# Optimization experiments

Hardware: AMD Instinct MI355X
Metric: run time of the kernel (lower is better)

## Reference

```python
import jax, jax.numpy as jnp
import numpy as np
from functools import partial

H = 51  # hidden size hard-coded in the module
B = 1024
T = 1024


def setup_inputs() -> dict:
    key = jax.random.key(0)
    ks = jax.random.split(key, 12)
    scale = 1.0 / np.sqrt(H)
    p = lambda k, shape: (jax.random.normal(k, shape, dtype=jnp.float32) * scale)
    return {
        "input": jax.random.normal(ks[0], (B, T), dtype=jnp.float32),
        # layer 1: LSTMCell(1, 51)
        "W_ih1": p(ks[1], (4 * H, 1)),
        "W_hh1": p(ks[2], (4 * H, H)),
        "b_ih1": p(ks[3], (4 * H,)),
        "b_hh1": p(ks[4], (4 * H,)),
        # layer 2: LSTMCell(51, 51)
        "W_ih2": p(ks[5], (4 * H, H)),
        "W_hh2": p(ks[6], (4 * H, H)),
        "b_ih2": p(ks[7], (4 * H,)),
        "b_hh2": p(ks[8], (4 * H,)),
        # Linear(51, 1)
        "W_lin": p(ks[9], (1, H)),
        "b_lin": p(ks[10], (1,)),
    }


def _lstm_cell(x, h, c, W_ih, W_hh, b_ih, b_hh):
    # PyTorch LSTMCell gate order: i, f, g, o
    gates = x @ W_ih.T + h @ W_hh.T + b_ih + b_hh  # [B, 4H]
    i, f, g, o = jnp.split(gates, 4, axis=-1)
    i = jax.nn.sigmoid(i)
    f = jax.nn.sigmoid(f)
    g = jnp.tanh(g)
    o = jax.nn.sigmoid(o)
    c_new = f * c + i * g
    h_new = o * jnp.tanh(c_new)
    return h_new, c_new


def reference(input, W_ih1, W_hh1, b_ih1, b_hh1, W_ih2, W_hh2, b_ih2, b_hh2, W_lin, b_lin):
    Bv = input.shape[0]
    dt = input.dtype
    init = (
        jnp.zeros((Bv, H), dt),  # h1
        jnp.zeros((Bv, H), dt),  # c1
        jnp.zeros((Bv, H), dt),  # h2
        jnp.zeros((Bv, H), dt),  # c2
    )

    def step(carry, x_t):  # x_t: [B, 1]
        h1, c1, h2, c2 = carry
        h1, c1 = _lstm_cell(x_t, h1, c1, W_ih1, W_hh1, b_ih1, b_hh1)
        h2, c2 = _lstm_cell(h1, h2, c2, W_ih2, W_hh2, b_ih2, b_hh2)
        y = h2 @ W_lin.T + b_lin  # [B, 1]
        return (h1, c1, h2, c2), y[:, 0]

    xs = input.T[:, :, None]  # [T, B, 1]
    _, ys = jax.lax.scan(step, init, xs)  # ys: [T, B]
    return ys.T  # [B, T]
```

## Files before the change

### kernel.cpp

```cpp
#include <hip/hip_runtime.h>


#define H     51
#define NROW  204
#define TLEN  1024
#define BPB   16
#define NTHR  896
#define NBLK  64
#define KPAD  88

#define LOG2E  1.442695041f
#define LOG2E2 2.885390082f

typedef __attribute__((ext_vector_type(8))) _Float16 half8;
typedef __attribute__((ext_vector_type(4))) float f4;

__device__ __forceinline__ float frcp(float x) { return __builtin_amdgcn_rcpf(x); }
#if __has_builtin(__builtin_amdgcn_exp2f)
__device__ __forceinline__ float ex2(float x) { return __builtin_amdgcn_exp2f(x); }
#else
__device__ __forceinline__ float ex2(float x) { return __expf(x * 0.6931471806f); }
#endif

__device__ __forceinline__ int posu(int u) {
    return (u & ~7) | ((u & 3) << 1) | ((u >> 2) & 1);
}
__device__ __forceinline__ int ipos(int p) {
    return (p & ~7) | ((p & 1) << 2) | ((p >> 1) & 3);
}

__device__ __forceinline__ half8 lds8h(const _Float16* p) {
    return *(const half8*)__builtin_assume_aligned(p, 16);
}

__device__ __forceinline__ void block_sync_lds() {
    asm volatile("s_waitcnt lgkmcnt(0)\n\ts_barrier" ::: "memory");
}

#define MFMA(ACC, A, B) \
    ACC = __builtin_amdgcn_mfma_f32_16x16x32_f16((A), (B), (ACC), 0, 0, 0)

__device__ __forceinline__ half8 load_wfrag(const float* __restrict__ W,
                                            int tile, int kt, int q, int mcol)
{
    half8 hf;
    const int prow = tile * 16 + mcol;
    const float sc = ((prow & 3) == 2) ? LOG2E2 : LOG2E;
#pragma unroll
    for (int j = 0; j < 8; ++j) {
        const int kk = ipos(kt * 32 + q * 8 + j);
        float v = 0.0f;
        if (prow < NROW && kk < H) {
            const int srow = (prow & 3) * H + (prow >> 2);
            v = W[srow * H + kk];
        }
        hf[j] = (_Float16)(v * sc);
    }
    return hf;
}

__device__ __forceinline__ float cell(float a_i, float a_f, float b_g,
                                      float d_o, float* c)
{
    const float e_i = ex2(-a_i);
    const float e_f = ex2(-a_f);
    const float Eg  = ex2(b_g);
    const float f   = frcp(1.0f + e_f);
    const float ig  = (Eg - 1.0f) * frcp((1.0f + e_i) * (Eg + 1.0f));
    const float cn  = fmaf(f, *c, ig);
    *c = cn;
    const float Ec  = ex2(cn * LOG2E2);
    const float e_o = ex2(-d_o);
    return (Ec - 1.0f) * frcp((Ec + 1.0f) * (1.0f + e_o));
}

__global__
__attribute__((amdgpu_flat_work_group_size(NTHR, NTHR), amdgpu_waves_per_eu(4, 4)))
void lstm2_kernel(const float* __restrict__ input,
                  const float* __restrict__ W_ih1, const float* __restrict__ W_hh1,
                  const float* __restrict__ b_ih1, const float* __restrict__ b_hh1,
                  const float* __restrict__ W_ih2, const float* __restrict__ W_hh2,
                  const float* __restrict__ b_ih2, const float* __restrict__ b_hh2,
                  const float* __restrict__ W_lin, const float* __restrict__ b_lin,
                  float* __restrict__ out)
{
    const int tid  = threadIdx.x;
    const int w    = tid >> 6;
    const int lane = tid & 63;
    const int q    = lane >> 4;
    const int mcol = lane & 15;
    const int b0   = blockIdx.x * BPB;

    const bool isL1 = (w < 7);
    const int  tw   = isL1 ? w : (w - 7);

    __shared__ __align__(16) _Float16 h1r[4][BPB][KPAD];
    __shared__ __align__(16) _Float16 h2r[2][BPB][KPAD];

    {
        _Float16* p1 = &h1r[0][0][0];
        for (int i = tid; i < 4 * BPB * KPAD; i += NTHR) p1[i] = (_Float16)0.0f;
        _Float16* p2 = &h2r[0][0][0];
        for (int i = tid; i < 2 * BPB * KPAD; i += NTHR) p2[i] = (_Float16)0.0f;
    }

    half8 Wa[2][2], Wb[2][2];
    f4 bbv[2], wxv[2];
    float cc[2] = {0.0f, 0.0f};
    int wp[2];
    const int tt[2] = {tw, 7 + tw};
#pragma unroll
    for (int s = 0; s < 2; ++s) {
        const int t = tt[s];
        const int u = 4 * t + q;
        wp[s] = posu(u);
#pragma unroll
        for (int kt = 0; kt < 2; ++kt) {
            if (isL1) {
                Wa[s][kt] = load_wfrag(W_hh1, t, kt, q, mcol);
            } else {
                Wa[s][kt] = load_wfrag(W_ih2, t, kt, q, mcol);
                Wb[s][kt] = load_wfrag(W_hh2, t, kt, q, mcol);
            }
        }
#pragma unroll
        for (int j = 0; j < 4; ++j) {
            const bool v = (t < 13) && (u < H);
            const float sc = (j == 2) ? LOG2E2 : LOG2E;
            if (isL1) {
                bbv[s][j] = v ? sc * (b_ih1[j * H + u] + b_hh1[j * H + u]) : 0.0f;
                wxv[s][j] = v ? sc * W_ih1[j * H + u] : 0.0f;
            } else {
                bbv[s][j] = v ? sc * (b_ih2[j * H + u] + b_hh2[j * H + u]) : 0.0f;
                wxv[s][j] = 0.0f;
            }
        }
    }

    float wl_a[8], wl_b[8];
    if (w == 7) {
#pragma unroll
        for (int j = 0; j < 8; ++j) {
            const int ra = ipos(q * 8 + j);
            const int rb = ipos(32 + q * 8 + j);
            wl_a[j] = (ra < H) ? W_lin[ra] : 0.0f;
            wl_b[j] = (rb < H) ? W_lin[rb] : 0.0f;
        }
    }
    const float blin = b_lin[0];

    float xcur = input[(size_t)(b0 + mcol) * TLEN + 0];
    half8 e1a = {0, 0, 0, 0, 0, 0, 0, 0};
    half8 e1b = {0, 0, 0, 0, 0, 0, 0, 0};

    __syncthreads();

#define STEP(KK, S1W, S1R, S2W, S2R, L1E, L2E, YE, ERE)                        \
do {                                                                           \
    const int k_ = (KK);                                                       \
    if (isL1) {                                                                \
        if (L1E) {                                                             \
            const int kn_ = (k_ + 1 < TLEN) ? (k_ + 1) : (TLEN - 1);           \
            const float xn_ = input[(size_t)(b0 + mcol) * TLEN + kn_];         \
            half8 B1a = lds8h(&h1r[S1R][mcol][q * 8]);                         \
            half8 B1b = lds8h(&h1r[S1R][mcol][32 + q * 8]);                    \
            f4 g0, g1;                                                         \
            g0[0] = fmaf(wxv[0][0], xcur, bbv[0][0]);                          \
            g0[1] = fmaf(wxv[0][1], xcur, bbv[0][1]);                          \
            g0[2] = fmaf(wxv[0][2], xcur, bbv[0][2]);                          \
            g0[3] = fmaf(wxv[0][3], xcur, bbv[0][3]);                          \
            g1[0] = fmaf(wxv[1][0], xcur, bbv[1][0]);                          \
            g1[1] = fmaf(wxv[1][1], xcur, bbv[1][1]);                          \
            g1[2] = fmaf(wxv[1][2], xcur, bbv[1][2]);                          \
            g1[3] = fmaf(wxv[1][3], xcur, bbv[1][3]);                          \
            MFMA(g0, Wa[0][0], B1a);  MFMA(g0, Wa[0][1], B1b);                 \
            MFMA(g1, Wa[1][0], B1a);  MFMA(g1, Wa[1][1], B1b);                 \
            const float h0 = cell(g0[0], g0[1], g0[2], g0[3], &cc[0]);         \
            const float h1v = cell(g1[0], g1[1], g1[2], g1[3], &cc[1]);        \
            h1r[S1W][mcol][wp[0]] = (_Float16)h0;                              \
            h1r[S1W][mcol][wp[1]] = (_Float16)h1v;                             \
            xcur = xn_;                                                        \
        }                                                                      \
    } else {                                                                   \
        if (L2E) {                                                             \
            half8 B2a = lds8h(&h2r[S2R][mcol][q * 8]);                         \
            half8 B2b = lds8h(&h2r[S2R][mcol][32 + q * 8]);                    \
            f4 g0 = bbv[0], g1 = bbv[1];                                       \
            MFMA(g0, Wa[0][0], e1a);  MFMA(g0, Wa[0][1], e1b);      \
            MFMA(g1, Wa[1][0], e1a);  MFMA(g1, Wa[1][1], e1b);                 \
            MFMA(g0, Wb[0][0], B2a);  MFMA(g0, Wb[0][1], B2b);                 \
            MFMA(g1, Wb[1][0], B2a);  MFMA(g1, Wb[1][1], B2b);                 \
            if (ERE) {             \
                e1a = lds8h(&h1r[S1R][mcol][q * 8]);                           \
                e1b = lds8h(&h1r[S1R][mcol][32 + q * 8]);                      \
            }                                                                  \
            const float h0 = cell(g0[0], g0[1], g0[2], g0[3], &cc[0]);         \
            const float h1v = cell(g1[0], g1[1], g1[2], g1[3], &cc[1]);        \
            h2r[S2W][mcol][wp[0]] = (_Float16)h0;                              \
            h2r[S2W][mcol][wp[1]] = (_Float16)h1v;                             \
            if ((YE) && w == 7) {    \
                float yp = 0.0f;                                               \
                _Pragma("unroll")                                              \
                for (int j = 0; j < 8; ++j) {                                  \
                    yp += wl_a[j] * (float)B2a[j];                             \
                    yp += wl_b[j] * (float)B2b[j];                             \
                }                                                              \
                yp += __shfl_xor(yp, 16);                                      \
                yp += __shfl_xor(yp, 32);                                      \
                if (q == 0) out[(size_t)(b0 + mcol) * TLEN + (k_ - 3)] = yp + blin; \
            }                                                                  \
        } else if (ERE) {                                                      \
            e1a = lds8h(&h1r[S1R][mcol][q * 8]);                               \
            e1b = lds8h(&h1r[S1R][mcol][32 + q * 8]);                          \
        }                                                                      \
    }                                                                          \
    block_sync_lds();                                                          \
} while (0)

    STEP(0, 0, 3, 0, 1, 1, 0, 0, 0);
    STEP(1, 1, 0, 1, 0, 1, 0, 0, 1);
    STEP(2, 2, 1, 0, 1, 1, 1, 0, 1);
    STEP(3, 3, 2, 1, 0, 1, 1, 1, 1);
    for (int k = 4; k <= 1020; k += 4) {
        STEP(k + 0, 0, 3, 0, 1, 1, 1, 1, 1);
        STEP(k + 1, 1, 0, 1, 0, 1, 1, 1, 1);
        STEP(k + 2, 2, 1, 0, 1, 1, 1, 1, 1);
        STEP(k + 3, 3, 2, 1, 0, 1, 1, 1, 1);
    }
    STEP(1024, 0, 3, 0, 1, 0, 1, 1, 1);
    STEP(1025, 1, 0, 1, 0, 0, 1, 1, 0);
#undef STEP

    if (w == 7) {
        half8 ya = lds8h(&h2r[1][mcol][q * 8]);
        half8 yb = lds8h(&h2r[1][mcol][32 + q * 8]);
        float yp = 0.0f;
#pragma unroll
        for (int j = 0; j < 8; ++j) {
            yp += wl_a[j] * (float)ya[j];
            yp += wl_b[j] * (float)yb[j];
        }
        yp += __shfl_xor(yp, 16);
        yp += __shfl_xor(yp, 32);
        if (q == 0) out[(size_t)(b0 + mcol) * TLEN + (TLEN - 1)] = yp + blin;
    }
}

extern "C" void kernel_launch(void* const* d_in, const int* in_sizes, int n_in,
                              void* d_out, int out_size, void* d_ws, size_t ws_size,
                              hipStream_t stream)
{
    const float* input = (const float*)d_in[0];
    const float* W_ih1 = (const float*)d_in[1];
    const float* W_hh1 = (const float*)d_in[2];
    const float* b_ih1 = (const float*)d_in[3];
    const float* b_hh1 = (const float*)d_in[4];
    const float* W_ih2 = (const float*)d_in[5];
    const float* W_hh2 = (const float*)d_in[6];
    const float* b_ih2 = (const float*)d_in[7];
    const float* b_hh2 = (const float*)d_in[8];
    const float* W_lin = (const float*)d_in[9];
    const float* b_lin = (const float*)d_in[10];

    float* out = (float*)d_out;

    hipLaunchKernelGGL(lstm2_kernel, dim3(NBLK), dim3(NTHR), 0, stream,
                       input, W_ih1, W_hh1, b_ih1, b_hh1,
                       W_ih2, W_hh2, b_ih2, b_hh2, W_lin, b_lin,
                       out);
}
```

Before: 724.2 us.

## Replace per-step block barriers with LDS counter flags between layer waves

Drops the block-wide barrier after every timestep. Layer-1 and layer-2 wave groups now signal progress through atomic counters in shared memory and spin with s_sleep until the data they need is ready. A 4-slot ring buffer for both hidden states lets layer 1 run up to a few steps ahead of layer 2, decoupling the two pipelines. This risks polling overhead, LDS atomic contention, and memory-ordering hazards, since writes are fenced only with lgkmcnt waits.

```diff
diff --git a/kernel.cpp b/kernel.cpp
--- a/kernel.cpp
+++ b/kernel.cpp
@@ -8,6 +8,7 @@
 #define NTHR  896
 #define NBLK  64
 #define KPAD  88
+#define RING  4
 
 #define LOG2E  1.442695041f
 #define LOG2E2 2.885390082f
@@ -31,10 +32,6 @@
 
 __device__ __forceinline__ half8 lds8h(const _Float16* p) {
     return *(const half8*)__builtin_assume_aligned(p, 16);
-}
-
-__device__ __forceinline__ void block_sync_lds() {
-    asm volatile("s_waitcnt lgkmcnt(0)\n\ts_barrier" ::: "memory");
 }
 
 #define MFMA(ACC, A, B) \
@@ -74,6 +71,14 @@
     return (Ec - 1.0f) * frcp((Ec + 1.0f) * (1.0f + e_o));
 }
 
+#define WAITGE(P, T)                                                           \
+do {                                                                           \
+    if (*(P) < (T)) {                                                          \
+        do { __builtin_amdgcn_s_sleep(1); } while (*(P) < (T));                \
+    }                                                                          \
+    __builtin_amdgcn_sched_barrier(0);                                         \
+} while (0)
+
 __global__
 __attribute__((amdgpu_flat_work_group_size(NTHR, NTHR), amdgpu_waves_per_eu(4, 4)))
 void lstm2_kernel(const float* __restrict__ input,
@@ -94,15 +99,19 @@
     const bool isL1 = (w < 7);
     const int  tw   = isL1 ? w : (w - 7);
 
-    __shared__ __align__(16) _Float16 h1r[4][BPB][KPAD];
-    __shared__ __align__(16) _Float16 h2r[2][BPB][KPAD];
+    __shared__ __align__(16) _Float16 h1r[RING][BPB][KPAD];
+    __shared__ __align__(16) _Float16 h2r[RING][BPB][KPAD];
+    __shared__ int dflag[16];
 
     {
         _Float16* p1 = &h1r[0][0][0];
-        for (int i = tid; i < 4 * BPB * KPAD; i += NTHR) p1[i] = (_Float16)0.0f;
+        for (int i = tid; i < RING * BPB * KPAD; i += NTHR) p1[i] = (_Float16)0.0f;
         _Float16* p2 = &h2r[0][0][0];
-        for (int i = tid; i < 2 * BPB * KPAD; i += NTHR) p2[i] = (_Float16)0.0f;
-    }
+        for (int i = tid; i < RING * BPB * KPAD; i += NTHR) p2[i] = (_Float16)0.0f;
+        if (tid < 16) dflag[tid] = 0;
+    }
+    volatile int* d1 = &dflag[0];
+    volatile int* d2 = &dflag[8];
 
     half8 Wa[2][2], Wb[2][2];
     f4 bbv[2], wxv[2];
@@ -149,101 +158,111 @@
     }
     const float blin = b_lin[0];
 
-    float xcur = input[(size_t)(b0 + mcol) * TLEN + 0];
-    half8 e1a = {0, 0, 0, 0, 0, 0, 0, 0};
-    half8 e1b = {0, 0, 0, 0, 0, 0, 0, 0};
+    float xcur = isL1 ? input[(size_t)(b0 + mcol) * TLEN + 0] : 0.0f;
 
     __syncthreads();
 
-#define STEP(KK, S1W, S1R, S2W, S2R, L1E, L2E, YE, ERE)                        \
+#define L1STEP(KK, SW, SR, W1, W2)                                             \
 do {                                                                           \
-    const int k_ = (KK);                                                       \
-    if (isL1) {                                                                \
-        if (L1E) {                                                             \
-            const int kn_ = (k_ + 1 < TLEN) ? (k_ + 1) : (TLEN - 1);           \
-            const float xn_ = input[(size_t)(b0 + mcol) * TLEN + kn_];         \
-            half8 B1a = lds8h(&h1r[S1R][mcol][q * 8]);                         \
-            half8 B1b = lds8h(&h1r[S1R][mcol][32 + q * 8]);                    \
-            f4 g0, g1;                                                         \
-            g0[0] = fmaf(wxv[0][0], xcur, bbv[0][0]);                          \
-            g0[1] = fmaf(wxv[0][1], xcur, bbv[0][1]);                          \
-            g0[2] = fmaf(wxv[0][2], xcur, bbv[0][2]);                          \
-            g0[3] = fmaf(wxv[0][3], xcur, bbv[0][3]);                          \
-            g1[0] = fmaf(wxv[1][0], xcur, bbv[1][0]);                          \
-            g1[1] = fmaf(wxv[1][1], xcur, bbv[1][1]);                          \
-            g1[2] = fmaf(wxv[1][2], xcur, bbv[1][2]);                          \
-            g1[3] = fmaf(wxv[1][3], xcur, bbv[1][3]);                          \
-            MFMA(g0, Wa[0][0], B1a);  MFMA(g0, Wa[0][1], B1b);                 \
-            MFMA(g1, Wa[1][0], B1a);  MFMA(g1, Wa[1][1], B1b);                 \
-            const float h0 = cell(g0[0], g0[1], g0[2], g0[3], &cc[0]);         \
-            const float h1v = cell(g1[0], g1[1], g1[2], g1[3], &cc[1]);        \
-            h1r[S1W][mcol][wp[0]] = (_Float16)h0;                              \
-            h1r[S1W][mcol][wp[1]] = (_Float16)h1v;                             \
-            xcur = xn_;                                                        \
+    const int k_  = (KK);                                                      \
+    const int kn_ = (k_ + 1 < TLEN) ? (k_ + 1) : (TLEN - 1);                   \
+    const float xn_ = input[(size_t)(b0 + mcol) * TLEN + kn_];                 \
+    if (W1) WAITGE(d1, 7 * k_);                                                \
+    if (W2) WAITGE(d2, 7 * (k_ - 3));                                          \
+    half8 B1a = lds8h(&h1r[SR][mcol][q * 8]);                                  \
+    half8 B1b = lds8h(&h1r[SR][mcol][32 + q * 8]);                             \
+    f4 g0, g1;                                                                 \
+    g0[0] = fmaf(wxv[0][0], xcur, bbv[0][0]);                                  \
+    g0[1] = fmaf(wxv[0][1], xcur, bbv[0][1]);                                  \
+    g0[2] = fmaf(wxv[0][2], xcur, bbv[0][2]);                                  \
+    g0[3] = fmaf(wxv[0][3], xcur, bbv[0][3]);                                  \
+    g1[0] = fmaf(wxv[1][0], xcur, bbv[1][0]);                                  \
+    g1[1] = fmaf(wxv[1][1], xcur, bbv[1][1]);                                  \
+    g1[2] = fmaf(wxv[1][2], xcur, bbv[1][2]);                                  \
+    g1[3] = fmaf(wxv[1][3], xcur, bbv[1][3]);                                  \
+    MFMA(g0, Wa[0][0], B1a);  MFMA(g0, Wa[0][1], B1b);                         \
+    MFMA(g1, Wa[1][0], B1a);  MFMA(g1, Wa[1][1], B1b);                         \
+    const float h0  = cell(g0[0], g0[1], g0[2], g0[3], &cc[0]);                \
+    const float h1v = cell(g1[0], g1[1], g1[2], g1[3], &cc[1]);                \
+    h1r[SW][mcol][wp[0]] = (_Float16)h0;                                       \
+    h1r[SW][mcol][wp[1]] = (_Float16)h1v;                                      \
+    asm volatile("s_waitcnt lgkmcnt(0)" ::: "memory");                         \
+    if (lane == 0) atomicAdd(&dflag[0], 1);                                    \
+    xcur = xn_;                                                                \
+} while (0)
+
+#define L2STEP(JJ, SW, SR2, W2, YE)                                            \
+do {                                                                           \
+    const int j_ = (JJ);                                                       \
+    WAITGE(d1, 7 * (j_ + 1));                                                  \
+    if (W2) WAITGE(d2, 7 * j_);                                                \
+    half8 B1a = lds8h(&h1r[SW][mcol][q * 8]);                                  \
+    half8 B1b = lds8h(&h1r[SW][mcol][32 + q * 8]);                             \
+    half8 B2a = lds8h(&h2r[SR2][mcol][q * 8]);                                 \
+    half8 B2b = lds8h(&h2r[SR2][mcol][32 + q * 8]);                            \
+    f4 g0 = bbv[0], g1 = bbv[1];                                               \
+    MFMA(g0, Wa[0][0], B1a);  MFMA(g0, Wa[0][1], B1b);                         \
+    MFMA(g1, Wa[1][0], B1a);  MFMA(g1, Wa[1][1], B1b);                         \
+    MFMA(g0, Wb[0][0], B2a);  MFMA(g0, Wb[0][1], B2b);                         \
+    MFMA(g1, Wb[1][0], B2a);  MFMA(g1, Wb[1][1], B2b);                         \
+    if ((YE) && w == 7) {                  \
+        float yp = 0.0f;                                                       \
+        _Pragma("unroll")                                                      \
+        for (int i = 0; i < 8; ++i) {                                          \
+            yp += wl_a[i] * (float)B2a[i];                                     \
+            yp += wl_b[i] * (float)B2b[i];                                     \
         }                                                                      \
-    } else {                                                                   \
-        if (L2E) {                                                             \
-            half8 B2a = lds8h(&h2r[S2R][mcol][q * 8]);                         \
-            half8 B2b = lds8h(&h2r[S2R][mcol][32 + q * 8]);                    \
-            f4 g0 = bbv[0], g1 = bbv[1];                                       \
-            MFMA(g0, Wa[0][0], e1a);  MFMA(g0, Wa[0][1], e1b);      \
-            MFMA(g1, Wa[1][0], e1a);  MFMA(g1, Wa[1][1], e1b);                 \
-            MFMA(g0, Wb[0][0], B2a);  MFMA(g0, Wb[0][1], B2b);                 \
-            MFMA(g1, Wb[1][0], B2a);  MFMA(g1, Wb[1][1], B2b);                 \
-            if (ERE) {             \
-                e1a = lds8h(&h1r[S1R][mcol][q * 8]);                           \
-                e1b = lds8h(&h1r[S1R][mcol][32 + q * 8]);                      \
-            }                                                                  \
-            const float h0 = cell(g0[0], g0[1], g0[2], g0[3], &cc[0]);         \
-            const float h1v = cell(g1[0], g1[1], g1[2], g1[3], &cc[1]);        \
-            h2r[S2W][mcol][wp[0]] = (_Float16)h0;                              \
-            h2r[S2W][mcol][wp[1]] = (_Float16)h1v;                             \
-            if ((YE) && w == 7) {    \
-                float yp = 0.0f;                                               \
-                _Pragma("unroll")                                              \
-                for (int j = 0; j < 8; ++j) {                                  \
-                    yp += wl_a[j] * (float)B2a[j];                             \
-                    yp += wl_b[j] * (float)B2b[j];                             \
-                }                                                              \
-                yp += __shfl_xor(yp, 16);                                      \
-                yp += __shfl_xor(yp, 32);                                      \
-                if (q == 0) out[(size_t)(b0 + mcol) * TLEN + (k_ - 3)] = yp + blin; \
-            }                                                                  \
-        } else if (ERE) {                                                      \
-            e1a = lds8h(&h1r[S1R][mcol][q * 8]);                               \
-            e1b = lds8h(&h1r[S1R][mcol][32 + q * 8]);                          \
-        }                                                                      \
+        yp += __shfl_xor(yp, 16);                                              \
+        yp += __shfl_xor(yp, 32);                                              \
+        if (q == 0) out[(size_t)(b0 + mcol) * TLEN + (j_ - 1)] = yp + blin;    \
     }                                                                          \
-    block_sync_lds();                                                          \
+    const float h0  = cell(g0[0], g0[1], g0[2], g0[3], &cc[0]);                \
+    const float h1v = cell(g1[0], g1[1], g1[2], g1[3], &cc[1]);                \
+    h2r[SW][mcol][wp[0]] = (_Float16)h0;                                       \
+    h2r[SW][mcol][wp[1]] = (_Float16)h1v;                                      \
+    asm volatile("s_waitcnt lgkmcnt(0)" ::: "memory");                         \
+    if (lane == 0) atomicAdd(&dflag[8], 1);                                    \
 } while (0)
 
-    STEP(0, 0, 3, 0, 1, 1, 0, 0, 0);
-    STEP(1, 1, 0, 1, 0, 1, 0, 0, 1);
-    STEP(2, 2, 1, 0, 1, 1, 1, 0, 1);
-    STEP(3, 3, 2, 1, 0, 1, 1, 1, 1);
-    for (int k = 4; k <= 1020; k += 4) {
-        STEP(k + 0, 0, 3, 0, 1, 1, 1, 1, 1);
-        STEP(k + 1, 1, 0, 1, 0, 1, 1, 1, 1);
-        STEP(k + 2, 2, 1, 0, 1, 1, 1, 1, 1);
-        STEP(k + 3, 3, 2, 1, 0, 1, 1, 1, 1);
-    }
-    STEP(1024, 0, 3, 0, 1, 0, 1, 1, 1);
-    STEP(1025, 1, 0, 1, 0, 0, 1, 1, 0);
-#undef STEP
-
-    if (w == 7) {
-        half8 ya = lds8h(&h2r[1][mcol][q * 8]);
-        half8 yb = lds8h(&h2r[1][mcol][32 + q * 8]);
-        float yp = 0.0f;
-#pragma unroll
-        for (int j = 0; j < 8; ++j) {
-            yp += wl_a[j] * (float)ya[j];
-            yp += wl_b[j] * (float)yb[j];
-        }
-        yp += __shfl_xor(yp, 16);
-        yp += __shfl_xor(yp, 32);
-        if (q == 0) out[(size_t)(b0 + mcol) * TLEN + (TLEN - 1)] = yp + blin;
-    }
+    if (isL1) {
+        L1STEP(0, 0, 3, 0, 0);
+        L1STEP(1, 1, 0, 1, 0);
+        L1STEP(2, 2, 1, 1, 0);
+        L1STEP(3, 3, 2, 1, 0);
+        for (int k = 4; k < TLEN; k += 4) {
+            L1STEP(k + 0, 0, 3, 1, 1);
+            L1STEP(k + 1, 1, 0, 1, 1);
+            L1STEP(k + 2, 2, 1, 1, 1);
+            L1STEP(k + 3, 3, 2, 1, 1);
+        }
+    } else {
+        L2STEP(0, 0, 3, 0, 0);
+        L2STEP(1, 1, 0, 1, 1);
+        L2STEP(2, 2, 1, 1, 1);
+        L2STEP(3, 3, 2, 1, 1);
+        for (int j = 4; j < TLEN; j += 4) {
+            L2STEP(j + 0, 0, 3, 1, 1);
+            L2STEP(j + 1, 1, 0, 1, 1);
+            L2STEP(j + 2, 2, 1, 1, 1);
+            L2STEP(j + 3, 3, 2, 1, 1);
+        }
+        if (w == 7) {
+            WAITGE(d2, 7 * TLEN);
+            half8 ya = lds8h(&h2r[3][mcol][q * 8]);
+            half8 yb = lds8h(&h2r[3][mcol][32 + q * 8]);
+            float yp = 0.0f;
+#pragma unroll
+            for (int i = 0; i < 8; ++i) {
+                yp += wl_a[i] * (float)ya[i];
+                yp += wl_b[i] * (float)yb[i];
+            }
+            yp += __shfl_xor(yp, 16);
+            yp += __shfl_xor(yp, 32);
+            if (q == 0) out[(size_t)(b0 + mcol) * TLEN + (TLEN - 1)] = yp + blin;
+        }
+    }
+#undef L1STEP
+#undef L2STEP
 }
 
 extern "C" void kernel_launch(void* const* d_in, const int* in_sizes, int n_in,
```

Measured after the change: 803.7 us. +11.0%, slower.

## Rebalance LSTM tiles across 16 waves with uneven per-wave tile assignment

Applied to the files above, without the earlier changes.

Raises the block from 14 to 16 waves, 8 for layer 1 and 8 for layer 2. Each wave gets one or two 16-row gate tiles from an explicit table, and the second tile's work is skipped when a wave owns only one. The goal is to spread the per-step MFMA and cell work over more waves and shorten the per-step critical path between barriers. The layer-2 output projection is also moved ahead of the cell updates. In exchange the barrier now covers more waves, the mapping mixes threads with one and two tiles, and the waves_per_eu attribute may no longer match 16 waves.

```diff
diff --git a/kernel.cpp b/kernel.cpp
--- a/kernel.cpp
+++ b/kernel.cpp
@@ -5,9 +5,10 @@
 #define NROW  204
 #define TLEN  1024
 #define BPB   16
-#define NTHR  896
+#define NTHR  1024
 #define NBLK  64
 #define KPAD  88
+#define RING  4
 
 #define LOG2E  1.442695041f
 #define LOG2E2 2.885390082f
@@ -91,15 +92,27 @@
     const int mcol = lane & 15;
     const int b0   = blockIdx.x * BPB;
 
-    const bool isL1 = (w < 7);
-    const int  tw   = isL1 ? w : (w - 7);
-
-    __shared__ __align__(16) _Float16 h1r[4][BPB][KPAD];
+    const bool isL1 = (w < 4) || (w >= 8 && w < 12);
+    int t0, t1;
+    bool has2;
+    if (isL1) {
+        const int i = (w < 4) ? w : (w - 4);
+        if (i < 4)      { t0 = 2 * i; t1 = 2 * i + 1; has2 = true; }
+        else if (i < 7) { t0 = 4 + i; t1 = 13;        has2 = false; }
+        else            { t0 = 11;    t1 = 12;        has2 = true;  }
+    } else {
+        const int i = (w < 8) ? (w - 4) : (w - 8);
+        if (i < 4)      { t0 = 2 * i; t1 = 2 * i + 1; has2 = true; }
+        else if (i == 4){ t0 = 8;     t1 = 12;        has2 = true;  }
+        else            { t0 = 4 + i; t1 = 13;        has2 = false; }
+    }
+    const bool y_wave = (w == 13);
+
+    __shared__ __align__(16) _Float16 h1r[RING][BPB][KPAD];
     __shared__ __align__(16) _Float16 h2r[2][BPB][KPAD];
-
     {
         _Float16* p1 = &h1r[0][0][0];
-        for (int i = tid; i < 4 * BPB * KPAD; i += NTHR) p1[i] = (_Float16)0.0f;
+        for (int i = tid; i < RING * BPB * KPAD; i += NTHR) p1[i] = (_Float16)0.0f;
         _Float16* p2 = &h2r[0][0][0];
         for (int i = tid; i < 2 * BPB * KPAD; i += NTHR) p2[i] = (_Float16)0.0f;
     }
@@ -108,7 +121,7 @@
     f4 bbv[2], wxv[2];
     float cc[2] = {0.0f, 0.0f};
     int wp[2];
-    const int tt[2] = {tw, 7 + tw};
+    const int tt[2] = {t0, t1};
 #pragma unroll
     for (int s = 0; s < 2; ++s) {
         const int t = tt[s];
@@ -138,7 +151,7 @@
     }
 
     float wl_a[8], wl_b[8];
-    if (w == 7) {
+    if (y_wave) {
 #pragma unroll
         for (int j = 0; j < 8; ++j) {
             const int ra = ipos(q * 8 + j);
@@ -149,7 +162,7 @@
     }
     const float blin = b_lin[0];
 
-    float xcur = input[(size_t)(b0 + mcol) * TLEN + 0];
+    float xcur = isL1 ? input[(size_t)(b0 + mcol) * TLEN + 0] : 0.0f;
     half8 e1a = {0, 0, 0, 0, 0, 0, 0, 0};
     half8 e1b = {0, 0, 0, 0, 0, 0, 0, 0};
 
@@ -164,50 +177,58 @@
             const float xn_ = input[(size_t)(b0 + mcol) * TLEN + kn_];         \
             half8 B1a = lds8h(&h1r[S1R][mcol][q * 8]);                         \
             half8 B1b = lds8h(&h1r[S1R][mcol][32 + q * 8]);                    \
-            f4 g0, g1;                                                         \
+            f4 g0;                                                             \
             g0[0] = fmaf(wxv[0][0], xcur, bbv[0][0]);                          \
             g0[1] = fmaf(wxv[0][1], xcur, bbv[0][1]);                          \
             g0[2] = fmaf(wxv[0][2], xcur, bbv[0][2]);                          \
             g0[3] = fmaf(wxv[0][3], xcur, bbv[0][3]);                          \
-            g1[0] = fmaf(wxv[1][0], xcur, bbv[1][0]);                          \
-            g1[1] = fmaf(wxv[1][1], xcur, bbv[1][1]);                          \
-            g1[2] = fmaf(wxv[1][2], xcur, bbv[1][2]);                          \
-            g1[3] = fmaf(wxv[1][3], xcur, bbv[1][3]);                          \
             MFMA(g0, Wa[0][0], B1a);  MFMA(g0, Wa[0][1], B1b);                 \
-            MFMA(g1, Wa[1][0], B1a);  MFMA(g1, Wa[1][1], B1b);                 \
             const float h0 = cell(g0[0], g0[1], g0[2], g0[3], &cc[0]);         \
-            const float h1v = cell(g1[0], g1[1], g1[2], g1[3], &cc[1]);        \
             h1r[S1W][mcol][wp[0]] = (_Float16)h0;                              \
-            h1r[S1W][mcol][wp[1]] = (_Float16)h1v;                             \
+            if (has2) {                                                        \
+                f4 g1;                                                         \
+                g1[0] = fmaf(wxv[1][0], xcur, bbv[1][0]);                      \
+                g1[1] = fmaf(wxv[1][1], xcur, bbv[1][1]);                      \
+                g1[2] = fmaf(wxv[1][2], xcur, bbv[1][2]);                      \
+                g1[3] = fmaf(wxv[1][3], xcur, bbv[1][3]);                      \
+                MFMA(g1, Wa[1][0], B1a);  MFMA(g1, Wa[1][1], B1b);             \
+                const float h1v = cell(g1[0], g1[1], g1[2], g1[3], &cc[1]);    \
+                h1r[S1W][mcol][wp[1]] = (_Float16)h1v;                         \
+            }                                                                  \
             xcur = xn_;                                                        \
         }                                                                      \
     } else {                                                                   \
         if (L2E) {                                                             \
             half8 B2a = lds8h(&h2r[S2R][mcol][q * 8]);                         \
             half8 B2b = lds8h(&h2r[S2R][mcol][32 + q * 8]);                    \
-            f4 g0 = bbv[0], g1 = bbv[1];                                       \
-            MFMA(g0, Wa[0][0], e1a);  MFMA(g0, Wa[0][1], e1b);      \
-            MFMA(g1, Wa[1][0], e1a);  MFMA(g1, Wa[1][1], e1b);                 \
+            f4 g0 = bbv[0];                                                    \
+            MFMA(g0, Wa[0][0], e1a);  MFMA(g0, Wa[0][1], e1b);                 \
             MFMA(g0, Wb[0][0], B2a);  MFMA(g0, Wb[0][1], B2b);                 \
-            MFMA(g1, Wb[1][0], B2a);  MFMA(g1, Wb[1][1], B2b);                 \
-            if (ERE) {             \
+            f4 g1 = bbv[1];                                                    \
+            if (has2) {                                                        \
+                MFMA(g1, Wa[1][0], e1a);  MFMA(g1, Wa[1][1], e1b);             \
+                MFMA(g1, Wb[1][0], B2a);  MFMA(g1, Wb[1][1], B2b);             \
+            }                                                                  \
+            if (ERE) {                  \
                 e1a = lds8h(&h1r[S1R][mcol][q * 8]);                           \
                 e1b = lds8h(&h1r[S1R][mcol][32 + q * 8]);                      \
             }                                                                  \
-            const float h0 = cell(g0[0], g0[1], g0[2], g0[3], &cc[0]);         \
-            const float h1v = cell(g1[0], g1[1], g1[2], g1[3], &cc[1]);        \
-            h2r[S2W][mcol][wp[0]] = (_Float16)h0;                              \
-            h2r[S2W][mcol][wp[1]] = (_Float16)h1v;                             \
-            if ((YE) && w == 7) {    \
+            if ((YE) && y_wave) {          \
                 float yp = 0.0f;                                               \
                 _Pragma("unroll")                                              \
-                for (int j = 0; j < 8; ++j) {                                  \
-                    yp += wl_a[j] * (float)B2a[j];                             \
-                    yp += wl_b[j] * (float)B2b[j];                             \
+                for (int i = 0; i < 8; ++i) {                                  \
+                    yp += wl_a[i] * (float)B2a[i];                             \
+                    yp += wl_b[i] * (float)B2b[i];                             \
                 }                                                              \
                 yp += __shfl_xor(yp, 16);                                      \
                 yp += __shfl_xor(yp, 32);                                      \
                 if (q == 0) out[(size_t)(b0 + mcol) * TLEN + (k_ - 3)] = yp + blin; \
+            }                                                                  \
+            const float h0 = cell(g0[0], g0[1], g0[2], g0[3], &cc[0]);         \
+            h2r[S2W][mcol][wp[0]] = (_Float16)h0;                              \
+            if (has2) {                                                        \
+                const float h1v = cell(g1[0], g1[1], g1[2], g1[3], &cc[1]);    \
+                h2r[S2W][mcol][wp[1]] = (_Float16)h1v;                         \
             }                                                                  \
         } else if (ERE) {                                                      \
             e1a = lds8h(&h1r[S1R][mcol][q * 8]);                               \
@@ -231,14 +252,14 @@
     STEP(1025, 1, 0, 1, 0, 0, 1, 1, 0);
 #undef STEP
 
-    if (w == 7) {
+    if (y_wave) {
         half8 ya = lds8h(&h2r[1][mcol][q * 8]);
         half8 yb = lds8h(&h2r[1][mcol][32 + q * 8]);
         float yp = 0.0f;
 #pragma unroll
-        for (int j = 0; j < 8; ++j) {
-            yp += wl_a[j] * (float)ya[j];
-            yp += wl_b[j] * (float)yb[j];
+        for (int i = 0; i < 8; ++i) {
+            yp += wl_a[i] * (float)ya[i];
+            yp += wl_b[i] * (float)yb[i];
         }
         yp += __shfl_xor(yp, 16);
         yp += __shfl_xor(yp, 32);
```

Measured after the change: 732.9 us. No clear change (+1.2%).
